# Kernel optimization log

Measured on AMD Instinct MI355X. Metric: run time of the kernel, lower is better.

The kernel has to match this reference:

```python
import jax, jax.numpy as jnp
import numpy as np

B, C, H, W = 2, 256, 96, 192
GROUPS = 4
K = 9  # search_window_1d = (1, 9) -> 9 candidates, x-offsets -4..4, y-offset 0


def bilinear_sample(img, coords):
    """F.grid_sample(mode='bilinear', padding_mode='zeros', align_corners=True)
    with absolute pixel coordinates (torchvision optical-flow grid_sample wrapper:
    normalize by 2*x/(W-1)-1 then grid_sample align_corners=True == identity mapping).
    img: [B, C, H, W]; coords: [B, Hg, Wg, 2] as (x, y). Returns [B, C, Hg, Wg]."""
    Bi, Ci, Hi, Wi = img.shape
    x = coords[..., 0]
    y = coords[..., 1]
    x0 = jnp.floor(x)
    y0 = jnp.floor(y)
    wx1 = x - x0
    wy1 = y - y0
    wx0 = 1.0 - wx1
    wy0 = 1.0 - wy1
    flat = img.reshape(Bi, Ci, Hi * Wi)

    def gather(ix, iy):
        valid = (ix >= 0) & (ix <= Wi - 1) & (iy >= 0) & (iy <= Hi - 1)
        ixc = jnp.clip(ix, 0, Wi - 1).astype(jnp.int32)
        iyc = jnp.clip(iy, 0, Hi - 1).astype(jnp.int32)
        idx = (iyc * Wi + ixc).reshape(Bi, 1, -1)  # [B,1,Hg*Wg]
        g = jnp.take_along_axis(flat, idx, axis=2)  # [B,C,Hg*Wg]
        g = g.reshape(Bi, Ci, *ix.shape[1:])
        return g * valid[:, None].astype(img.dtype)

    out = (gather(x0, y0) * (wx0 * wy0)[:, None]
           + gather(x0 + 1, y0) * (wx1 * wy0)[:, None]
           + gather(x0, y0 + 1) * (wx0 * wy1)[:, None]
           + gather(x0 + 1, y0 + 1) * (wx1 * wy1)[:, None])
    return out


def setup_inputs() -> dict:
    key = jax.random.key(0)
    k1, k2, k3, k4 = jax.random.split(key, 4)
    return {
        "left_feature": jax.random.normal(k1, (B, C, H, W), dtype=jnp.float32),
        "right_feature": jax.random.normal(k2, (B, C, H, W), dtype=jnp.float32),
        "flow": jax.random.normal(k3, (B, 2, H, W), dtype=jnp.float32),
        "extra_offset": jax.random.normal(k4, (B, 2 * K, H, W), dtype=jnp.float32),
    }


def reference(left_feature, right_feature, flow, extra_offset):
    Bf, Cf, Hf, Wf = left_feature.shape
    gc = Cf // GROUPS
    dt = left_feature.dtype
    # 1d window offsets: meshgrid(arange(-4,5), arange(0,1), 'xy') -> (x, 0) pairs
    xs = jnp.arange(-4, 5, dtype=dt)
    win_offs = jnp.stack([xs, jnp.zeros_like(xs)], axis=-1)  # [K,2] (x,y)
    # extra_offset: [B, K, 2, H, W] -> [B, K, H, W, 2]
    extra = extra_offset.reshape(Bf, K, 2, Hf, Wf).transpose(0, 1, 3, 4, 2)
    offsets = win_offs[None, :, None, None, :] + extra  # [B,K,H,W,2]
    # base coords grid (x, y) + flow
    yy, xx = jnp.meshgrid(jnp.arange(Hf), jnp.arange(Wf), indexing="ij")
    base = jnp.stack([xx, yy], axis=-1).astype(dt)  # [H,W,2]
    coords = base[None] + flow.transpose(0, 2, 3, 1)  # [B,H,W,2]
    coords = coords[:, None] + offsets  # [B,K,H,W,2]
    coords = coords.reshape(Bf, K * Hf, Wf, 2)
    # All groups share identical window/dilation -> sample full right feature once.
    sampled = bilinear_sample(right_feature, coords)  # [B,C,K*H,W]
    sampled = sampled.reshape(Bf, GROUPS, gc, K, Hf, Wf)
    left = left_feature.reshape(Bf, GROUPS, gc, 1, Hf, Wf)
    corr = jnp.mean(left * sampled, axis=2)  # [B,G,K,H,W]
    return corr.reshape(Bf, GROUPS * K, Hf, Wf)
```

## Files before the change

### kernel.cpp

```cpp
#include <hip/hip_runtime.h>


namespace {
constexpr int kB = 2;
constexpr int kC = 256;
constexpr int kH = 96;
constexpr int kW = 192;
constexpr int kG = 4;
constexpr int kGC = kC / kG;
constexpr int kK = 9;
constexpr int kHW = kH * kW;
constexpr size_t kPlane = (size_t)kC * kHW;
constexpr int kTransBlocks = (kHW / 64) * (kC / 64) * kB * 2;
constexpr int kCorrBlocks  = kB * kHW / 8;
}

typedef _Float16 half8_t __attribute__((ext_vector_type(8)));
typedef _Float16 half4_t __attribute__((ext_vector_type(4)));
typedef _Float16 half2_t __attribute__((ext_vector_type(2)));

struct TapMeta {
  int4   off;
  float4 wgt;
};

__device__ __forceinline__ float dot8(half8_t a, half8_t b, float acc) {
#if __has_builtin(__builtin_amdgcn_fdot2)
  #pragma unroll
  for (int i = 0; i < 4; ++i) {
    half2_t a2 = {a[2 * i], a[2 * i + 1]};
    half2_t b2 = {b[2 * i], b[2 * i + 1]};
    acc = __builtin_amdgcn_fdot2(a2, b2, acc, false);
  }
#else
  #pragma unroll
  for (int i = 0; i < 8; ++i) acc += (float)a[i] * (float)b[i];
#endif
  return acc;
}

__global__ __launch_bounds__(256) void prepass_kernel(
    const float* __restrict__ left, const float* __restrict__ right,
    _Float16* __restrict__ left_t, _Float16* __restrict__ right_t)
{
  __shared__ float tile[64][65];
  int tb = blockIdx.x;
  int pt = tb % (kHW / 64);
  int ct = (tb / (kHW / 64)) % 4;
  int z  = tb / ((kHW / 64) * 4);
  int b  = z >> 1;
  const float* in = (z & 1) ? right : left;
  _Float16*   dst = (z & 1) ? right_t : left_t;
  int p0 = pt * 64, c0 = ct * 64;
  const float* inb = in + (size_t)b * kPlane;
  _Float16*   outb = dst + (size_t)b * kPlane;
  int t = threadIdx.x;
  int cl = t >> 2;
  int q  = t & 3;
  #pragma unroll
  for (int i = 0; i < 4; ++i) {
    int j = q + 4 * i;
    float4 v = *(const float4*)(inb + (size_t)(c0 + cl) * kHW + p0 + 4 * j);
    tile[cl][4 * j + 0] = v.x;
    tile[cl][4 * j + 1] = v.y;
    tile[cl][4 * j + 2] = v.z;
    tile[cl][4 * j + 3] = v.w;
  }
  __syncthreads();
  int pl8 = t >> 3;
  int c8  = t & 7;
  #pragma unroll
  for (int i = 0; i < 2; ++i) {
    int px = pl8 + 32 * i;
    half8_t hv;
    #pragma unroll
    for (int j = 0; j < 8; ++j)
      hv[j] = (_Float16)tile[8 * c8 + j][px];
    *(half8_t*)(outb + (size_t)(p0 + px) * kC + c0 + 8 * c8) = hv;
  }
}

__global__ __launch_bounds__(256) void corr_fp16_kernel(
    const _Float16* __restrict__ left_t, const _Float16* __restrict__ right_t,
    const float* __restrict__ flow, const float* __restrict__ extra,
    float* __restrict__ out)
{
  __shared__ TapMeta smeta[8 * kK];

  int sb = (blockIdx.x & 7) * (kCorrBlocks / 8) + (blockIdx.x >> 3);
  int blockPix = sb * 8;
  int b    = blockPix / kHW;
  int pix0 = blockPix % kHW;

  int wv   = threadIdx.x >> 6;
  int lane = threadIdx.x & 63;
  int p    = lane >> 5;
  int cl   = lane & 31;
  int pix  = pix0 + wv * 2 + p;

  half8_t l8 = *(const half8_t*)(left_t + ((size_t)b * kHW + pix) * kC + cl * 8);

  int t = threadIdx.x;
  if (t < 8 * kK) {
    int px = t / kK;
    int k  = t - px * kK;
    int gpix = pix0 + px;
    int w = gpix % kW, h = gpix / kW;

    const float* flowb = flow + (size_t)b * 2 * kHW + gpix;
    float bx = (float)w + flowb[0];
    float by = (float)h + flowb[kHW];
    const float* extb = extra + (size_t)b * 2 * kK * kHW + gpix;

    float xx = bx + (float)(k - 4) + extb[(size_t)(2 * k) * kHW];
    float yy = by + extb[(size_t)(2 * k + 1) * kHW];
    float xf = floorf(xx), yf = floorf(yy);
    float fx = xx - xf, fy = yy - yf;
    int ix0 = (int)xf, iy0 = (int)yf;
    int ix1 = ix0 + 1, iy1 = iy0 + 1;
    bool vx0 = (ix0 >= 0) && (ix0 < kW);
    bool vx1 = (ix1 >= 0) && (ix1 < kW);
    bool vy0 = (iy0 >= 0) && (iy0 < kH);
    bool vy1 = (iy1 >= 0) && (iy1 < kH);
    int xc0 = min(max(ix0, 0), kW - 1);
    int xc1 = min(max(ix1, 0), kW - 1);
    int yc0 = min(max(iy0, 0), kH - 1);
    int yc1 = min(max(iy1, 0), kH - 1);
    float wx0 = 1.f - fx, wy0 = 1.f - fy;
    TapMeta m;
    m.off.x = (yc0 * kW + xc0) * kC;
    m.off.y = (yc0 * kW + xc1) * kC;
    m.off.z = (yc1 * kW + xc0) * kC;
    m.off.w = (yc1 * kW + xc1) * kC;
    m.wgt.x = wx0 * wy0 * ((vx0 && vy0) ? 1.f : 0.f);
    m.wgt.y = fx  * wy0 * ((vx1 && vy0) ? 1.f : 0.f);
    m.wgt.z = wx0 * fy  * ((vx0 && vy1) ? 1.f : 0.f);
    m.wgt.w = fx  * fy  * ((vx1 && vy1) ? 1.f : 0.f);
    smeta[t] = m;
  }

  const _Float16* Rb = right_t + (size_t)b * kPlane + cl * 8;

  __syncthreads();
  const TapMeta* mp = smeta + (wv * 2 + p) * kK;

  float rr[kK];

  #pragma unroll
  for (int kb = 0; kb < kK; kb += 3) {
    int4   off[3];
    float4 wv4[3];
    #pragma unroll
    for (int j = 0; j < 3; ++j) {
      off[j] = mp[kb + j].off;
      wv4[j] = mp[kb + j].wgt;
    }
    half8_t tp[3][4];
    #pragma unroll
    for (int j = 0; j < 3; ++j) {
      tp[j][0] = *(const half8_t*)(Rb + off[j].x);
      tp[j][1] = *(const half8_t*)(Rb + off[j].y);
      tp[j][2] = *(const half8_t*)(Rb + off[j].z);
      tp[j][3] = *(const half8_t*)(Rb + off[j].w);
    }
    #pragma unroll
    for (int j = 0; j < 3; ++j) {
      float d00 = dot8(tp[j][0], l8, 0.f);
      float d01 = dot8(tp[j][1], l8, 0.f);
      float d10 = dot8(tp[j][2], l8, 0.f);
      float d11 = dot8(tp[j][3], l8, 0.f);
      float r = wv4[j].x * d00 + wv4[j].y * d01 + wv4[j].z * d10 + wv4[j].w * d11;
      r += __shfl_xor(r, 1);
      r += __shfl_xor(r, 2);
      r += __shfl_xor(r, 4);
      rr[kb + j] = r;
    }
  }

  int g = cl >> 3;
  if ((cl & 7) == 0) {
    float* outp = out + ((size_t)b * kG + g) * kK * kHW + pix;
    #pragma unroll
    for (int k = 0; k < kK; ++k)
      outp[(size_t)k * kHW] = rr[k] * (1.f / kGC);
  }
}

__global__ __launch_bounds__(256) void crestereo_corr_fallback(
    const float* __restrict__ left, const float* __restrict__ right,
    const float* __restrict__ flow, const float* __restrict__ extra,
    float* __restrict__ out)
{
  int t = blockIdx.x * blockDim.x + threadIdx.x;
  int w = t % kW;
  int h = (t / kW) % kH;
  int k = (t / kHW) % kK;
  int g = (t / (kHW * kK)) % kG;
  int b = t / (kHW * kK * kG);

  int pix = h * kW + w;
  const float* flowb = flow + b * 2 * kHW + pix;
  float x = (float)(w + (k - 4)) + flowb[0];
  float y = (float)h + flowb[kHW];
  const float* extb = extra + (size_t)(b * 2 * kK + 2 * k) * kHW + pix;
  x += extb[0];
  y += extb[kHW];

  float xf = floorf(x), yf = floorf(y);
  float fx = x - xf, fy = y - yf;
  int ix0 = (int)xf, iy0 = (int)yf;
  int ix1 = ix0 + 1, iy1 = iy0 + 1;
  bool vx0 = (ix0 >= 0) && (ix0 < kW);
  bool vx1 = (ix1 >= 0) && (ix1 < kW);
  bool vy0 = (iy0 >= 0) && (iy0 < kH);
  bool vy1 = (iy1 >= 0) && (iy1 < kH);
  int xc0 = min(max(ix0, 0), kW - 1);
  int xc1 = min(max(ix1, 0), kW - 1);
  int yc0 = min(max(iy0, 0), kH - 1);
  int yc1 = min(max(iy1, 0), kH - 1);
  float wx0 = 1.f - fx, wy0 = 1.f - fy;
  float w00 = wx0 * wy0 * ((vx0 && vy0) ? 1.f : 0.f);
  float w01 = fx  * wy0 * ((vx1 && vy0) ? 1.f : 0.f);
  float w10 = wx0 * fy  * ((vx0 && vy1) ? 1.f : 0.f);
  float w11 = fx  * fy  * ((vx1 && vy1) ? 1.f : 0.f);
  int idx = yc0 * kW + xc0;
  int dx  = xc1 - xc0;
  int dyw = (yc1 - yc0) * kW;

  const float* Rb = right + (size_t)(b * kC + g * kGC) * kHW + idx;
  const float* Lb = left  + (size_t)(b * kC + g * kGC) * kHW + pix;

  float acc = 0.f;
  #pragma unroll 4
  for (int c = 0; c < kGC; ++c) {
    const float* Rc = Rb + (size_t)c * kHW;
    float l   = Lb[(size_t)c * kHW];
    acc += l * (w00 * Rc[0] + w01 * Rc[dx] + w10 * Rc[dyw] + w11 * Rc[dx + dyw]);
  }
  out[(size_t)((b * kG + g) * kK + k) * kHW + pix] = acc * (1.f / kGC);
}

extern "C" void kernel_launch(void* const* d_in, const int* in_sizes, int n_in,
                              void* d_out, int out_size, void* d_ws, size_t ws_size,
                              hipStream_t stream) {
  const float* left  = (const float*)d_in[0];
  const float* right = (const float*)d_in[1];
  const float* flow  = (const float*)d_in[2];
  const float* extra = (const float*)d_in[3];
  float* out = (float*)d_out;

  size_t t_bytes = 2 * (size_t)kB * kPlane * sizeof(_Float16);
  if (ws_size >= t_bytes) {
    _Float16* left_t  = (_Float16*)d_ws;
    _Float16* right_t = left_t + (size_t)kB * kPlane;

    prepass_kernel<<<kTransBlocks, 256, 0, stream>>>(left, right, left_t, right_t);
    corr_fp16_kernel<<<kCorrBlocks, 256, 0, stream>>>(
        left_t, right_t, flow, extra, out);
  } else {
    int total = kB * kG * kK * kH * kW;
    crestereo_corr_fallback<<<(total + 255) / 256, 256, 0, stream>>>(
        left, right, flow, extra, out);
  }
}
```

Baseline: 138.6 us.

## Fuse left-feature transpose into correlation kernel via shared memory

The prepass now transposes only the right feature to channel-last fp16. The correlation kernel reads the left feature directly in its original fp32 NCHW layout: each thread loads 8 consecutive pixels for one channel, converts them to fp16 and stages them in shared memory. This drops half of the prepass work and one fp16 intermediate write and read. In exchange the left loads become 32-byte segments strided by a full plane per channel, and shared memory now holds an extra per-block left tile.

```diff
diff --git a/kernel.cpp b/kernel.cpp
--- a/kernel.cpp
+++ b/kernel.cpp
@@ -11,7 +11,7 @@
 constexpr int kK = 9;
 constexpr int kHW = kH * kW;
 constexpr size_t kPlane = (size_t)kC * kHW;
-constexpr int kTransBlocks = (kHW / 64) * (kC / 64) * kB * 2;
+constexpr int kTransBlocks = (kHW / 64) * (kC / 64) * kB;
 constexpr int kCorrBlocks  = kB * kHW / 8;
 }
 
@@ -40,20 +40,16 @@
 }
 
 __global__ __launch_bounds__(256) void prepass_kernel(
-    const float* __restrict__ left, const float* __restrict__ right,
-    _Float16* __restrict__ left_t, _Float16* __restrict__ right_t)
+    const float* __restrict__ right, _Float16* __restrict__ right_t)
 {
   __shared__ float tile[64][65];
   int tb = blockIdx.x;
   int pt = tb % (kHW / 64);
   int ct = (tb / (kHW / 64)) % 4;
-  int z  = tb / ((kHW / 64) * 4);
-  int b  = z >> 1;
-  const float* in = (z & 1) ? right : left;
-  _Float16*   dst = (z & 1) ? right_t : left_t;
+  int b  = tb / ((kHW / 64) * 4);
   int p0 = pt * 64, c0 = ct * 64;
-  const float* inb = in + (size_t)b * kPlane;
-  _Float16*   outb = dst + (size_t)b * kPlane;
+  const float* inb = right + (size_t)b * kPlane;
+  _Float16*   outb = right_t + (size_t)b * kPlane;
   int t = threadIdx.x;
   int cl = t >> 2;
   int q  = t & 3;
@@ -81,26 +77,24 @@
 }
 
 __global__ __launch_bounds__(256) void corr_fp16_kernel(
-    const _Float16* __restrict__ left_t, const _Float16* __restrict__ right_t,
+    const _Float16* __restrict__ right_t, const float* __restrict__ left,
     const float* __restrict__ flow, const float* __restrict__ extra,
     float* __restrict__ out)
 {
   __shared__ TapMeta smeta[8 * kK];
+  __shared__ _Float16 smleft[8][kC];
 
   int sb = (blockIdx.x & 7) * (kCorrBlocks / 8) + (blockIdx.x >> 3);
   int blockPix = sb * 8;
   int b    = blockPix / kHW;
   int pix0 = blockPix % kHW;
 
-  int wv   = threadIdx.x >> 6;
-  int lane = threadIdx.x & 63;
-  int p    = lane >> 5;
-  int cl   = lane & 31;
-  int pix  = pix0 + wv * 2 + p;
-
-  half8_t l8 = *(const half8_t*)(left_t + ((size_t)b * kHW + pix) * kC + cl * 8);
-
   int t = threadIdx.x;
+
+  const float* Lb = left + (size_t)b * kPlane + (size_t)t * kHW + pix0;
+  float4 lv0 = *(const float4*)(Lb);
+  float4 lv1 = *(const float4*)(Lb + 4);
+
   if (t < 8 * kK) {
     int px = t / kK;
     int k  = t - px * kK;
@@ -139,9 +133,24 @@
     smeta[t] = m;
   }
 
+  {
+    float lv[8] = {lv0.x, lv0.y, lv0.z, lv0.w, lv1.x, lv1.y, lv1.z, lv1.w};
+    #pragma unroll
+    for (int j = 0; j < 8; ++j)
+      smleft[j][t] = (_Float16)lv[j];
+  }
+
+  int wv   = t >> 6;
+  int lane = t & 63;
+  int p    = lane >> 5;
+  int cl   = lane & 31;
+  int pix  = pix0 + wv * 2 + p;
+
   const _Float16* Rb = right_t + (size_t)b * kPlane + cl * 8;
 
   __syncthreads();
+
+  half8_t l8 = *(const half8_t*)&smleft[wv * 2 + p][cl * 8];
   const TapMeta* mp = smeta + (wv * 2 + p) * kK;
 
   float rr[kK];
@@ -249,14 +258,13 @@
   const float* extra = (const float*)d_in[3];
   float* out = (float*)d_out;
 
-  size_t t_bytes = 2 * (size_t)kB * kPlane * sizeof(_Float16);
+  size_t t_bytes = (size_t)kB * kPlane * sizeof(_Float16);
   if (ws_size >= t_bytes) {
-    _Float16* left_t  = (_Float16*)d_ws;
-    _Float16* right_t = left_t + (size_t)kB * kPlane;
-
-    prepass_kernel<<<kTransBlocks, 256, 0, stream>>>(left, right, left_t, right_t);
+    _Float16* right_t = (_Float16*)d_ws;
+
+    prepass_kernel<<<kTransBlocks, 256, 0, stream>>>(right, right_t);
     corr_fp16_kernel<<<kCorrBlocks, 256, 0, stream>>>(
-        left_t, right_t, flow, extra, out);
+        right_t, left, flow, extra, out);
   } else {
     int total = kB * kG * kK * kH * kW;
     crestereo_corr_fallback<<<(total + 255) / 256, 256, 0, stream>>>(
```

After: 138.1 us. Within noise of the previous version (-0.4%).
